# Performance work log

Hardware: AMD Instinct MI355X
Metric: run time of the kernel (lower is better)

The kernel has to match this reference:

```python
import jax, jax.numpy as jnp
import numpy as np

N = 4096      # particles
E = 262144    # interacting pairs (~64 neighbors each)
H = 128       # MLP hidden width
FD = 6        # force/velocity DOF (force + torque)
FEAT = 7      # rel(3) + dist + r_sq + r_quad + min_dist
IN_DIM = FEAT + 2 * FD  # 19


def setup_inputs() -> dict:
    key = jax.random.key(0)
    ks = jax.random.split(key, 10)
    rel_vecs = jax.random.normal(ks[0], (N, N, 3), jnp.float32)
    target_indices = jax.random.randint(ks[1], (E,), 0, N, dtype=jnp.int64)
    source_indices = jax.random.randint(ks[2], (E,), 0, N, dtype=jnp.int64)
    force = jax.random.normal(ks[3], (N, FD), jnp.float32)
    viscosity = jnp.ones((1,), jnp.float32)
    s1 = 1.0 / np.sqrt(IN_DIM)
    s2 = 1.0 / np.sqrt(H)
    W1 = jax.random.normal(ks[4], (IN_DIM, H), jnp.float32) * s1
    b1 = jnp.zeros((H,), jnp.float32)
    W2 = jax.random.normal(ks[5], (H, H), jnp.float32) * s2
    b2 = jnp.zeros((H,), jnp.float32)
    W3 = jax.random.normal(ks[6], (H, FD), jnp.float32) * s2
    b3 = jnp.zeros((FD,), jnp.float32)
    median = jnp.float32(2.5)
    contact_distance = jnp.float32(2.0)
    return {
        'rel_vecs': rel_vecs, 'target_indices': target_indices,
        'source_indices': source_indices, 'force': force,
        'viscosity': viscosity, 'median': median,
        'contact_distance': contact_distance,
        'W1': W1, 'b1': b1, 'W2': W2, 'b2': b2, 'W3': W3, 'b3': b3,
    }


def _predict_velocity(features, f_t, f_s, mu, W1, b1, W2, b2, W3, b3):
    # MLP over concatenated pair features + both forces; Stokes flow is
    # linear in force/viscosity, so scale output by 1/mu.
    x = jnp.concatenate([features, f_t, f_s], axis=-1)  # [E, 19]
    h = jax.nn.relu(x @ W1 + b1)
    h = jax.nn.relu(h @ W2 + b2)
    return (h @ W3 + b3) / mu  # [E, FD]


def reference(rel_vecs, target_indices, source_indices, force, viscosity,
              median, contact_distance, W1, b1, W2, b2, W3, b3):
    # Gather pairwise relative vectors: [E, 3]
    rel_selected = rel_vecs[target_indices, source_indices]
    dist = jnp.maximum(
        jnp.linalg.norm(rel_selected, axis=-1, keepdims=True), 1e-8)  # [E,1]
    r_shift = dist - median
    r_sq = r_shift * r_shift
    r_quad = r_sq * r_sq
    min_dist = dist - contact_distance
    features = jnp.concatenate(
        [rel_selected, dist, r_sq, r_quad, min_dist], axis=-1)  # [E, 7]
    force_target = force[target_indices]  # [E, FD]
    force_source = force[source_indices]  # [E, FD]
    mu = jnp.asarray(viscosity, dtype=force.dtype).reshape(())
    vel = _predict_velocity(features, force_target, force_source, mu,
                            W1, b1, W2, b2, W3, b3)  # [E, FD]
    # Scatter-add per-target contributions
    contribution = jnp.zeros_like(force).at[target_indices].add(vel)
    return contribution
```

## Files before the change

### kernel.cpp

```cpp
#include <hip/hip_runtime.h>

#define NPART 4096
#define E_TOT 262144
#define HID   128
#define FDOF  6
#define BM    64
#define NIT   (E_TOT / BM)
#define GRID  1024
#define XPAD  40
#define HPAD  136

typedef __bf16 bf16x8 __attribute__((ext_vector_type(8)));
typedef float  f32x4  __attribute__((ext_vector_type(4)));

__global__ void pairvel_zero_kernel(float* __restrict__ out, int n) {
    const int i = blockIdx.x * blockDim.x + threadIdx.x;
    if (i < n) out[i] = 0.0f;
}

__global__ __launch_bounds__(256) void pairvel_mfma_kernel(
    const float* __restrict__ rel,
    const int*   __restrict__ tgt,
    const int*   __restrict__ src,
    const float* __restrict__ force,
    const float* __restrict__ visc,
    const float* __restrict__ medianp,
    const float* __restrict__ contactp,
    const float* __restrict__ W1,
    const float* __restrict__ b1,
    const float* __restrict__ W2,
    const float* __restrict__ b2,
    const float* __restrict__ W3,
    const float* __restrict__ b3,
    float* __restrict__ out)
{
    const int tid = threadIdx.x;
    const int w   = tid >> 6;
    const int l   = tid & 63;
    const int l15 = l & 15;
    const int lhi = l >> 4;

    bf16x8 w1f[2], w2f[4][2], w3f[4];
    #pragma unroll
    for (int nb = 0; nb < 2; ++nb) {
        const int n = (2 * w + nb) * 16 + l15;
        #pragma unroll
        for (int r = 0; r < 8; ++r) {
            const int k = lhi * 8 + r;
            w1f[nb][r] = (k < 19) ? (__bf16)W1[k * HID + n] : (__bf16)0.0f;
        }
    }
    #pragma unroll
    for (int kt = 0; kt < 4; ++kt)
        #pragma unroll
        for (int nb = 0; nb < 2; ++nb) {
            const int n = (2 * w + nb) * 16 + l15;
            #pragma unroll
            for (int r = 0; r < 8; ++r)
                w2f[kt][nb][r] = (__bf16)W2[(kt * 32 + lhi * 8 + r) * HID + n];
        }
    #pragma unroll
    for (int kt = 0; kt < 4; ++kt)
        #pragma unroll
        for (int r = 0; r < 8; ++r) {
            const int k = kt * 32 + lhi * 8 + r;
            w3f[kt][r] = (l15 < FDOF) ? (__bf16)W3[k * FDOF + l15] : (__bf16)0.0f;
        }

    const float b1v0 = b1[(2 * w) * 16 + l15];
    const float b1v1 = b1[(2 * w + 1) * 16 + l15];
    const float b2v0 = b2[(2 * w) * 16 + l15];
    const float b2v1 = b2[(2 * w + 1) * 16 + l15];
    const float b3v  = (l15 < FDOF) ? b3[l15] : 0.0f;
    const float inv_mu  = 1.0f / visc[0];
    const float median  = medianp[0];
    const float contact = contactp[0];

    __shared__ __align__(16) __bf16 Xs[2][BM][XPAD];
    __shared__ __align__(16) __bf16 Hs[BM][HPAD];
    __shared__ int tgts[2][BM];

    for (int t = tid; t < 2 * BM * 13; t += 256) {
        const int b = t / (BM * 13), rem = t % (BM * 13);
        Xs[b][rem / 13][19 + rem % 13] = (__bf16)0.0f;
    }

    int   p_i0 = 0;
    float p_v0 = 0.f, p_v1 = 0.f, p_v2 = 0.f;
    float p_f3 = 0.f, p_f4 = 0.f, p_f5 = 0.f;

    auto gather_load = [&](int e0n) {
        if (tid < BM) {
            const int eg = e0n + tid;
            p_i0 = tgt[eg];
            const int sg = src[eg];
            const float* rp = rel + ((size_t)p_i0 * NPART + sg) * 3;
            p_v0 = rp[0]; p_v1 = rp[1]; p_v2 = rp[2];
        } else if (tid < 2 * BM) {
            const int eg = e0n + (tid - BM);
            const float2* f2 =
                reinterpret_cast<const float2*>(force + (size_t)tgt[eg] * FDOF);
            const float2 u0 = f2[0], u1 = f2[1], u2 = f2[2];
            p_v0 = u0.x; p_v1 = u0.y; p_v2 = u1.x;
            p_f3 = u1.y; p_f4 = u2.x; p_f5 = u2.y;
        } else if (tid < 3 * BM) {
            const int eg = e0n + (tid - 2 * BM);
            const float2* f2 =
                reinterpret_cast<const float2*>(force + (size_t)src[eg] * FDOF);
            const float2 u0 = f2[0], u1 = f2[1], u2 = f2[2];
            p_v0 = u0.x; p_v1 = u0.y; p_v2 = u1.x;
            p_f3 = u1.y; p_f4 = u2.x; p_f5 = u2.y;
        }
    };

    auto write_x = [&](int b) {
        if (tid < BM) {
            const int e = tid;
            tgts[b][e] = p_i0;
            const float dist = fmaxf(
                sqrtf(p_v0 * p_v0 + p_v1 * p_v1 + p_v2 * p_v2), 1e-8f);
            const float rs = (dist - median) * (dist - median);
            Xs[b][e][0] = (__bf16)p_v0;
            Xs[b][e][1] = (__bf16)p_v1;
            Xs[b][e][2] = (__bf16)p_v2;
            Xs[b][e][3] = (__bf16)dist;
            Xs[b][e][4] = (__bf16)rs;
            Xs[b][e][5] = (__bf16)(rs * rs);
            Xs[b][e][6] = (__bf16)(dist - contact);
        } else if (tid < 2 * BM) {
            const int e = tid - BM;
            Xs[b][e][7]  = (__bf16)p_v0;
            Xs[b][e][8]  = (__bf16)p_v1;
            Xs[b][e][9]  = (__bf16)p_v2;
            Xs[b][e][10] = (__bf16)p_f3;
            Xs[b][e][11] = (__bf16)p_f4;
            Xs[b][e][12] = (__bf16)p_f5;
        } else if (tid < 3 * BM) {
            const int e = tid - 2 * BM;
            Xs[b][e][13] = (__bf16)p_v0;
            Xs[b][e][14] = (__bf16)p_v1;
            Xs[b][e][15] = (__bf16)p_v2;
            Xs[b][e][16] = (__bf16)p_f3;
            Xs[b][e][17] = (__bf16)p_f4;
            Xs[b][e][18] = (__bf16)p_f5;
        }
    };

    gather_load(blockIdx.x * BM);
    write_x(0);
    if (blockIdx.x + GRID < NIT) gather_load((blockIdx.x + GRID) * BM);
    int buf = 0;

    for (int it = blockIdx.x; it < NIT; it += GRID) {
        __syncthreads();

        #pragma unroll
        for (int m = 0; m < 4; ++m) {
            const bf16x8 a = *reinterpret_cast<const bf16x8*>(
                &Xs[buf][m * 16 + l15][lhi * 8]);
            #pragma unroll
            for (int nb = 0; nb < 2; ++nb) {
                const float bv = nb ? b1v1 : b1v0;
                f32x4 acc = { bv, bv, bv, bv };
                acc = __builtin_amdgcn_mfma_f32_16x16x32_bf16(
                          a, w1f[nb], acc, 0, 0, 0);
                #pragma unroll
                for (int r = 0; r < 4; ++r)
                    Hs[m * 16 + lhi * 4 + r][(2 * w + nb) * 16 + l15] =
                        (__bf16)fmaxf(acc[r], 0.0f);
            }
        }
        __syncthreads();

        f32x4 accs[4][2];
        #pragma unroll
        for (int m = 0; m < 4; ++m) {
            accs[m][0] = (f32x4){ b2v0, b2v0, b2v0, b2v0 };
            accs[m][1] = (f32x4){ b2v1, b2v1, b2v1, b2v1 };
            #pragma unroll
            for (int kt = 0; kt < 4; ++kt) {
                const bf16x8 a = *reinterpret_cast<const bf16x8*>(
                    &Hs[m * 16 + l15][kt * 32 + lhi * 8]);
                accs[m][0] = __builtin_amdgcn_mfma_f32_16x16x32_bf16(
                                 a, w2f[kt][0], accs[m][0], 0, 0, 0);
                accs[m][1] = __builtin_amdgcn_mfma_f32_16x16x32_bf16(
                                 a, w2f[kt][1], accs[m][1], 0, 0, 0);
            }
        }
        __syncthreads();

        #pragma unroll
        for (int m = 0; m < 4; ++m)
            #pragma unroll
            for (int nb = 0; nb < 2; ++nb)
                #pragma unroll
                for (int r = 0; r < 4; ++r)
                    Hs[m * 16 + lhi * 4 + r][(2 * w + nb) * 16 + l15] =
                        (__bf16)fmaxf(accs[m][nb][r], 0.0f);

        if (it + GRID < NIT) write_x(buf ^ 1);
        if (it + 2 * GRID < NIT)
            gather_load((it + 2 * GRID) * BM);
        __syncthreads();

        f32x4 acc3 = { 0.0f, 0.0f, 0.0f, 0.0f };
        #pragma unroll
        for (int kt = 0; kt < 4; ++kt) {
            const bf16x8 a = *reinterpret_cast<const bf16x8*>(
                &Hs[w * 16 + l15][kt * 32 + lhi * 8]);
            acc3 = __builtin_amdgcn_mfma_f32_16x16x32_bf16(
                       a, w3f[kt], acc3, 0, 0, 0);
        }
        if (l15 < FDOF) {
            #pragma unroll
            for (int r = 0; r < 4; ++r) {
                const int e = w * 16 + lhi * 4 + r;
                atomicAdd(&out[(size_t)tgts[buf][e] * FDOF + l15],
                          (acc3[r] + b3v) * inv_mu);
            }
        }
        buf ^= 1;
    }
}

extern "C" void kernel_launch(void* const* d_in, const int* in_sizes, int n_in,
                              void* d_out, int out_size, void* d_ws, size_t ws_size,
                              hipStream_t stream) {
    const float* rel   = (const float*)d_in[0];
    const int*   tgt   = (const int*)d_in[1];
    const int*   src   = (const int*)d_in[2];
    const float* force = (const float*)d_in[3];
    const float* visc  = (const float*)d_in[4];
    const float* med   = (const float*)d_in[5];
    const float* con   = (const float*)d_in[6];
    const float* W1    = (const float*)d_in[7];
    const float* b1    = (const float*)d_in[8];
    const float* W2    = (const float*)d_in[9];
    const float* b2    = (const float*)d_in[10];
    const float* W3    = (const float*)d_in[11];
    const float* b3    = (const float*)d_in[12];
    float* out = (float*)d_out;

    pairvel_zero_kernel<<<(out_size + 255) / 256, 256, 0, stream>>>(out, out_size);
    pairvel_mfma_kernel<<<GRID, 256, 0, stream>>>(
        rel, tgt, src, force, visc, med, con, W1, b1, W2, b2, W3, b3, out);
}
```

Before: 49.35 us.

## Transpose MFMA operands for vectorized LDS stores and reorder input features

The MFMA operand order is swapped so weights are the A operand and activations the B operand. Each lane then holds four consecutive hidden units for one edge and can write them to shared memory as one 4-wide store instead of four scattered scalar stores. The input feature columns are permuted, with W1 rows remapped to match, so the gathered force and geometry values are written with vector stores. The prefetch distance is cut from two iterations to one, with the gather moved to after layer 1. This trims LDS store instructions and register pressure but may expose more global-gather latency.

```diff
diff --git a/kernel.cpp b/kernel.cpp
--- a/kernel.cpp
+++ b/kernel.cpp
@@ -11,6 +11,8 @@
 #define HPAD  136
 
 typedef __bf16 bf16x8 __attribute__((ext_vector_type(8)));
+typedef __bf16 bf16x4 __attribute__((ext_vector_type(4)));
+typedef __bf16 bf16x2 __attribute__((ext_vector_type(2)));
 typedef float  f32x4  __attribute__((ext_vector_type(4)));
 
 __global__ void pairvel_zero_kernel(float* __restrict__ out, int n) {
@@ -47,7 +49,8 @@
         #pragma unroll
         for (int r = 0; r < 8; ++r) {
             const int k = lhi * 8 + r;
-            w1f[nb][r] = (k < 19) ? (__bf16)W1[k * HID + n] : (__bf16)0.0f;
+            const int ko = (k < 12) ? k + 7 : k - 12;
+            w1f[nb][r] = (k < 19) ? (__bf16)W1[ko * HID + n] : (__bf16)0.0f;
         }
     }
     #pragma unroll
@@ -67,11 +70,20 @@
             w3f[kt][r] = (l15 < FDOF) ? (__bf16)W3[k * FDOF + l15] : (__bf16)0.0f;
         }
 
-    const float b1v0 = b1[(2 * w) * 16 + l15];
-    const float b1v1 = b1[(2 * w + 1) * 16 + l15];
-    const float b2v0 = b2[(2 * w) * 16 + l15];
-    const float b2v1 = b2[(2 * w + 1) * 16 + l15];
-    const float b3v  = (l15 < FDOF) ? b3[l15] : 0.0f;
+    f32x4 b1i[2], b2i[2];
+    #pragma unroll
+    for (int nb = 0; nb < 2; ++nb) {
+        b1i[nb] = *reinterpret_cast<const f32x4*>(
+            &b1[(2 * w + nb) * 16 + lhi * 4]);
+        b2i[nb] = *reinterpret_cast<const f32x4*>(
+            &b2[(2 * w + nb) * 16 + lhi * 4]);
+    }
+    float b3r[4];
+    #pragma unroll
+    for (int r = 0; r < 4; ++r) {
+        const int d = lhi * 4 + r;
+        b3r[r] = (d < FDOF) ? b3[d] : 0.0f;
+    }
     const float inv_mu  = 1.0f / visc[0];
     const float median  = medianp[0];
     const float contact = contactp[0];
@@ -120,103 +132,105 @@
             const float dist = fmaxf(
                 sqrtf(p_v0 * p_v0 + p_v1 * p_v1 + p_v2 * p_v2), 1e-8f);
             const float rs = (dist - median) * (dist - median);
-            Xs[b][e][0] = (__bf16)p_v0;
-            Xs[b][e][1] = (__bf16)p_v1;
-            Xs[b][e][2] = (__bf16)p_v2;
-            Xs[b][e][3] = (__bf16)dist;
-            Xs[b][e][4] = (__bf16)rs;
-            Xs[b][e][5] = (__bf16)(rs * rs);
-            Xs[b][e][6] = (__bf16)(dist - contact);
+            bf16x4 g0 = { (__bf16)p_v0, (__bf16)p_v1,
+                          (__bf16)p_v2, (__bf16)dist };
+            *reinterpret_cast<bf16x4*>(&Xs[b][e][12]) = g0;
+            bf16x2 g1 = { (__bf16)rs, (__bf16)(rs * rs) };
+            *reinterpret_cast<bf16x2*>(&Xs[b][e][16]) = g1;
+            Xs[b][e][18] = (__bf16)(dist - contact);
         } else if (tid < 2 * BM) {
             const int e = tid - BM;
-            Xs[b][e][7]  = (__bf16)p_v0;
-            Xs[b][e][8]  = (__bf16)p_v1;
-            Xs[b][e][9]  = (__bf16)p_v2;
-            Xs[b][e][10] = (__bf16)p_f3;
-            Xs[b][e][11] = (__bf16)p_f4;
-            Xs[b][e][12] = (__bf16)p_f5;
+            bf16x4 g0 = { (__bf16)p_v0, (__bf16)p_v1,
+                          (__bf16)p_v2, (__bf16)p_f3 };
+            *reinterpret_cast<bf16x4*>(&Xs[b][e][0]) = g0;
+            bf16x2 g1 = { (__bf16)p_f4, (__bf16)p_f5 };
+            *reinterpret_cast<bf16x2*>(&Xs[b][e][4]) = g1;
         } else if (tid < 3 * BM) {
             const int e = tid - 2 * BM;
-            Xs[b][e][13] = (__bf16)p_v0;
-            Xs[b][e][14] = (__bf16)p_v1;
-            Xs[b][e][15] = (__bf16)p_v2;
-            Xs[b][e][16] = (__bf16)p_f3;
-            Xs[b][e][17] = (__bf16)p_f4;
-            Xs[b][e][18] = (__bf16)p_f5;
+            bf16x2 g0 = { (__bf16)p_v0, (__bf16)p_v1 };
+            *reinterpret_cast<bf16x2*>(&Xs[b][e][6]) = g0;
+            bf16x4 g1 = { (__bf16)p_v2, (__bf16)p_f3,
+                          (__bf16)p_f4, (__bf16)p_f5 };
+            *reinterpret_cast<bf16x4*>(&Xs[b][e][8]) = g1;
         }
     };
 
     gather_load(blockIdx.x * BM);
     write_x(0);
-    if (blockIdx.x + GRID < NIT) gather_load((blockIdx.x + GRID) * BM);
     int buf = 0;
 
     for (int it = blockIdx.x; it < NIT; it += GRID) {
         __syncthreads();
 
         #pragma unroll
-        for (int m = 0; m < 4; ++m) {
-            const bf16x8 a = *reinterpret_cast<const bf16x8*>(
-                &Xs[buf][m * 16 + l15][lhi * 8]);
+        for (int et = 0; et < 4; ++et) {
+            const bf16x8 xb = *reinterpret_cast<const bf16x8*>(
+                &Xs[buf][et * 16 + l15][lhi * 8]);
             #pragma unroll
             for (int nb = 0; nb < 2; ++nb) {
-                const float bv = nb ? b1v1 : b1v0;
-                f32x4 acc = { bv, bv, bv, bv };
+                f32x4 acc = b1i[nb];
                 acc = __builtin_amdgcn_mfma_f32_16x16x32_bf16(
-                          a, w1f[nb], acc, 0, 0, 0);
+                          w1f[nb], xb, acc, 0, 0, 0);
+                bf16x4 hv;
                 #pragma unroll
                 for (int r = 0; r < 4; ++r)
-                    Hs[m * 16 + lhi * 4 + r][(2 * w + nb) * 16 + l15] =
-                        (__bf16)fmaxf(acc[r], 0.0f);
-            }
-        }
-        __syncthreads();
+                    hv[r] = (__bf16)fmaxf(acc[r], 0.0f);
+                *reinterpret_cast<bf16x4*>(
+                    &Hs[et * 16 + l15][(2 * w + nb) * 16 + lhi * 4]) = hv;
+            }
+        }
+        __syncthreads();
+
+        const bool havenext = (it + GRID) < NIT;
+        if (havenext) gather_load((it + GRID) * BM);
 
         f32x4 accs[4][2];
         #pragma unroll
-        for (int m = 0; m < 4; ++m) {
-            accs[m][0] = (f32x4){ b2v0, b2v0, b2v0, b2v0 };
-            accs[m][1] = (f32x4){ b2v1, b2v1, b2v1, b2v1 };
+        for (int et = 0; et < 4; ++et) {
+            accs[et][0] = b2i[0];
+            accs[et][1] = b2i[1];
             #pragma unroll
             for (int kt = 0; kt < 4; ++kt) {
-                const bf16x8 a = *reinterpret_cast<const bf16x8*>(
-                    &Hs[m * 16 + l15][kt * 32 + lhi * 8]);
-                accs[m][0] = __builtin_amdgcn_mfma_f32_16x16x32_bf16(
-                                 a, w2f[kt][0], accs[m][0], 0, 0, 0);
-                accs[m][1] = __builtin_amdgcn_mfma_f32_16x16x32_bf16(
-                                 a, w2f[kt][1], accs[m][1], 0, 0, 0);
-            }
-        }
-        __syncthreads();
-
-        #pragma unroll
-        for (int m = 0; m < 4; ++m)
-            #pragma unroll
-            for (int nb = 0; nb < 2; ++nb)
+                const bf16x8 hb = *reinterpret_cast<const bf16x8*>(
+                    &Hs[et * 16 + l15][kt * 32 + lhi * 8]);
+                accs[et][0] = __builtin_amdgcn_mfma_f32_16x16x32_bf16(
+                                  w2f[kt][0], hb, accs[et][0], 0, 0, 0);
+                accs[et][1] = __builtin_amdgcn_mfma_f32_16x16x32_bf16(
+                                  w2f[kt][1], hb, accs[et][1], 0, 0, 0);
+            }
+        }
+        __syncthreads();
+
+        #pragma unroll
+        for (int et = 0; et < 4; ++et)
+            #pragma unroll
+            for (int nb = 0; nb < 2; ++nb) {
+                bf16x4 hv;
                 #pragma unroll
                 for (int r = 0; r < 4; ++r)
-                    Hs[m * 16 + lhi * 4 + r][(2 * w + nb) * 16 + l15] =
-                        (__bf16)fmaxf(accs[m][nb][r], 0.0f);
-
-        if (it + GRID < NIT) write_x(buf ^ 1);
-        if (it + 2 * GRID < NIT)
-            gather_load((it + 2 * GRID) * BM);
+                    hv[r] = (__bf16)fmaxf(accs[et][nb][r], 0.0f);
+                *reinterpret_cast<bf16x4*>(
+                    &Hs[et * 16 + l15][(2 * w + nb) * 16 + lhi * 4]) = hv;
+            }
+        if (havenext) write_x(buf ^ 1);
         __syncthreads();
 
         f32x4 acc3 = { 0.0f, 0.0f, 0.0f, 0.0f };
         #pragma unroll
         for (int kt = 0; kt < 4; ++kt) {
-            const bf16x8 a = *reinterpret_cast<const bf16x8*>(
+            const bf16x8 hb = *reinterpret_cast<const bf16x8*>(
                 &Hs[w * 16 + l15][kt * 32 + lhi * 8]);
             acc3 = __builtin_amdgcn_mfma_f32_16x16x32_bf16(
-                       a, w3f[kt], acc3, 0, 0, 0);
-        }
-        if (l15 < FDOF) {
+                       w3f[kt], hb, acc3, 0, 0, 0);
+        }
+        if (lhi < 2) {
+            const int tg = tgts[buf][w * 16 + l15];
             #pragma unroll
             for (int r = 0; r < 4; ++r) {
-                const int e = w * 16 + lhi * 4 + r;
-                atomicAdd(&out[(size_t)tgts[buf][e] * FDOF + l15],
-                          (acc3[r] + b3v) * inv_mu);
+                const int d = lhi * 4 + r;
+                if (d < FDOF)
+                    atomicAdd(&out[(size_t)tg * FDOF + d],
+                              (acc3[r] + b3r[r]) * inv_mu);
             }
         }
         buf ^= 1;
```

After: 89.63 us. 81.6% more time.
